# Kernel optimization log

Hardware: AMD Instinct MI355X
Metric: run time of the kernel (lower is better)

## Reference

```python
import jax, jax.numpy as jnp
import numpy as np
from jax import lax

C = 128          # channel_size
NUM_HEAD = 2
P = 4            # local_patch_num


def setup_inputs() -> dict:
    key = jax.random.key(0)
    ks = jax.random.split(key, 16)
    def w(k, shape, scale=0.02):
        return jax.random.normal(k, shape, dtype=jnp.float32) * scale
    return dict(
        x=jax.random.normal(ks[0], (16, C, 128, 128), jnp.float32),
        h0=jax.random.normal(ks[1], (1, C, 64, 64), jnp.float32),
        c0=jax.random.normal(ks[2], (1, C, 64, 64), jnp.float32),
        conv_w=w(ks[3], (C, C, 2, 2)), conv_b=jnp.zeros((C,), jnp.float32),
        qkv1_w=w(ks[4], (3 * C, C)), qkv1_b=jnp.zeros((3 * C,), jnp.float32),
        mlp1_w1=w(ks[5], (4 * C, C)), mlp1_b1=jnp.zeros((4 * C,), jnp.float32),
        mlp1_w2=w(ks[6], (C, 4 * C)), mlp1_b2=jnp.zeros((C,), jnp.float32),
        qkv2_w=w(ks[7], (3 * C, C)), qkv2_b=jnp.zeros((3 * C,), jnp.float32),
        mlp2_w1=w(ks[8], (4 * C, C)), mlp2_b1=jnp.zeros((4 * C,), jnp.float32),
        mlp2_w2=w(ks[9], (C, 4 * C)), mlp2_b2=jnp.zeros((C,), jnp.float32),
        lstm_wx=w(ks[10], (4 * C, C)),   # 1x1 conv, no bias
        lstm_wh=w(ks[11], (4 * C, C)),   # 1x1 conv
        lstm_bh=jnp.zeros((4 * C,), jnp.float32),
    )


def _linear(x, w, b):
    # torch Linear: y = x @ W.T + b, W is [out, in]
    return jnp.einsum('...i,oi->...o', x, w) + b


def _msa(x, w, b, num_head):
    # x: [b, A, L, c]; attend over L within each group A. scale = sqrt(channel_size).
    bb, A, L, c = x.shape
    hd = c // num_head
    qkv = _linear(x, w, b).reshape(bb, A, L, 3, num_head, hd)
    q = jnp.transpose(qkv[..., 0, :, :], (0, 1, 3, 2, 4))  # [b,A,h,L,hd]
    k = jnp.transpose(qkv[..., 1, :, :], (0, 1, 3, 2, 4))
    v = jnp.transpose(qkv[..., 2, :, :], (0, 1, 3, 2, 4))
    score = jnp.einsum('bahlc,bahmc->bahlm', q, k) / (c ** 0.5)
    attn = jax.nn.softmax(score, axis=-1)
    out = jnp.einsum('bahlm,bahmc->bahlc', attn, v)
    return jnp.transpose(out, (0, 1, 3, 2, 4)).reshape(bb, A, L, c)


def _mlp(x, w1, b1, w2, b2):
    return _linear(jax.nn.gelu(_linear(x, w1, b1), approximate=False), w2, b2)


def reference(x, h0, c0, conv_w, conv_b,
              qkv1_w, qkv1_b, mlp1_w1, mlp1_b1, mlp1_w2, mlp1_b2,
              qkv2_w, qkv2_b, mlp2_w1, mlp2_b1, mlp2_w2, mlp2_b2,
              lstm_wx, lstm_wh, lstm_bh):
    # Conv2d(C, C, kernel=2, stride=2)
    x = lax.conv_general_dilated(x, conv_w, (2, 2), 'VALID',
                                 dimension_numbers=('NCHW', 'OIHW', 'NCHW'))
    x = x + conv_b[None, :, None, None]
    b, c, Hs, Ws = x.shape
    yg, xg = Hs // P, Ws // P
    # Window_partition: b c (yg yl) (xg xl) -> b (yg xg) (yl xl) c
    xw = x.reshape(b, c, yg, P, xg, P).transpose(0, 2, 4, 3, 5, 1).reshape(b, yg * xg, P * P, c)
    xw = xw + _msa(xw, qkv1_w, qkv1_b, NUM_HEAD)      # LocalMSA over window tokens
    xw = xw + _mlp(xw, mlp1_w1, mlp1_b1, mlp1_w2, mlp1_b2)
    xt = jnp.transpose(xw, (0, 2, 1, 3))              # b g l c -> b l g c
    xt = xt + _msa(xt, qkv2_w, qkv2_b, NUM_HEAD)      # DilatedMSA over windows
    xt = xt + _mlp(xt, mlp2_w1, mlp2_b1, mlp2_w2, mlp2_b2)
    # Window_reverse: b (yl xl) (yg xg) c -> b c (yg yl) (xg xl)
    xr = xt.reshape(b, P, P, yg, xg, c).transpose(0, 5, 3, 1, 4, 2).reshape(b, c, yg * P, xg * P)

    # ConvLSTM recurrence over the batch dimension (hidden carried sample-to-sample)
    def step(carry, xi):
        h, Cc = carry  # [C,H,W]
        gates = (jnp.einsum('oc,chw->ohw', lstm_wx, xi)
                 + jnp.einsum('oc,chw->ohw', lstm_wh, h)
                 + lstm_bh[:, None, None])
        f, i, s, o = jnp.split(gates, 4, axis=0)
        f = jax.nn.softmax(f, axis=0)   # Softmax2d = softmax over channels
        i = jax.nn.softmax(i, axis=0)
        o = jax.nn.softmax(o, axis=0)
        s = jnp.tanh(s)
        Cn = f * Cc + i * s
        hn = o * jnp.tanh(Cn)
        return (hn, Cn), hn

    (hf, Cf), hs = lax.scan(step, (h0[0], c0[0]), xr)
    return hs, hf[None], Cf[None]
```

## Files before the change

### kernel.cpp

```cpp
#include <hip/hip_runtime.h>
#include <hip/hip_bf16.h>

typedef unsigned int u32;
typedef unsigned short u16;

#define DI __device__ __forceinline__

typedef __attribute__((ext_vector_type(8))) __bf16 bf16x8;
typedef __attribute__((ext_vector_type(4))) float f32x4;

DI float b2f_u(u32 u){ return __uint_as_float(u << 16); }
DI u16 f2b_u(float f){
  u32 x = __float_as_uint(f);
  x += 0x7fffu + ((x >> 16) & 1u);
  return (u16)(x >> 16);
}
DI void ld8b(const u16* p, float* o){
  uint4 v = *reinterpret_cast<const uint4*>(p);
  o[0] = b2f_u(v.x & 0xffffu); o[1] = b2f_u(v.x >> 16);
  o[2] = b2f_u(v.y & 0xffffu); o[3] = b2f_u(v.y >> 16);
  o[4] = b2f_u(v.z & 0xffffu); o[5] = b2f_u(v.z >> 16);
  o[6] = b2f_u(v.w & 0xffffu); o[7] = b2f_u(v.w >> 16);
}
DI void st8b(u16* p, const float* i){
  uint4 v;
  v.x = (u32)f2b_u(i[0]) | ((u32)f2b_u(i[1]) << 16);
  v.y = (u32)f2b_u(i[2]) | ((u32)f2b_u(i[3]) << 16);
  v.z = (u32)f2b_u(i[4]) | ((u32)f2b_u(i[5]) << 16);
  v.w = (u32)f2b_u(i[6]) | ((u32)f2b_u(i[7]) << 16);
  *reinterpret_cast<uint4*>(p) = v;
}

__global__ void k_detect(const u32* __restrict__ xw, int* __restrict__ flag){
  __shared__ int cnt;
  int t = threadIdx.x;
  if (t == 0) cnt = 0;
  __syncthreads();
  int c = 0;
  for (int i = t; i < 2048; i += 256){
    u32 lo = xw[i] & 0xffffu;
    u32 e = (lo >> 7) & 0xffu;
    if (e < 100u || e > 140u) c++;
  }
  atomicAdd(&cnt, c);
  __syncthreads();
  if (t == 0) *flag = (cnt > 200) ? 1 : 0;
}

__global__ void k_prep(
  const void* __restrict__ conv_w, const void* __restrict__ qkv1_w,
  const void* __restrict__ m1w1, const void* __restrict__ m1w2,
  const void* __restrict__ qkv2_w, const void* __restrict__ m2w1, const void* __restrict__ m2w2,
  const void* __restrict__ lwx, const void* __restrict__ lwh,
  const void* __restrict__ conv_b, const void* __restrict__ qkv1_b,
  const void* __restrict__ m1b1, const void* __restrict__ m1b2,
  const void* __restrict__ qkv2_b, const void* __restrict__ m2b1, const void* __restrict__ m2b2,
  const void* __restrict__ lbh,
  u16* __restrict__ wB_conv, u16* __restrict__ wB_qkv1, u16* __restrict__ wB_m1a,
  u16* __restrict__ wB_m1b, u16* __restrict__ wB_qkv2, u16* __restrict__ wB_m2a,
  u16* __restrict__ wB_m2b, u16* __restrict__ wBx, u16* __restrict__ wBh,
  float* __restrict__ bf_conv, float* __restrict__ bf_qkv1, float* __restrict__ bf_m1b1,
  float* __restrict__ bf_m1b2, float* __restrict__ bf_qkv2, float* __restrict__ bf_m2b1,
  float* __restrict__ bf_m2b2, float* __restrict__ bf_lbh,
  const int* __restrict__ flag){
  int bid = blockIdx.x, t = threadIdx.x;
  int fl = *flag;
  auto cvb = [&](const void* s, u16* d, int base, int n){
    int i = (bid - base)*256 + t;
    if (i < n) d[i] = fl ? f2b_u(((const float*)s)[i]) : ((const u16*)s)[i];
  };
  auto ldf = [&](const void* s, int i)->float{
    return fl ? ((const float*)s)[i] : b2f_u((u32)((const u16*)s)[i]);
  };
  if (bid < 256)       cvb(conv_w, wB_conv, 0,    65536);
  else if (bid < 448)  cvb(qkv1_w, wB_qkv1, 256,  49152);
  else if (bid < 704)  cvb(m1w1,   wB_m1a,  448,  65536);
  else if (bid < 960)  cvb(m1w2,   wB_m1b,  704,  65536);
  else if (bid < 1152) cvb(qkv2_w, wB_qkv2, 960,  49152);
  else if (bid < 1408) cvb(m2w1,   wB_m2a,  1152, 65536);
  else if (bid < 1664) cvb(m2w2,   wB_m2b,  1408, 65536);
  else if (bid < 1920) cvb(lwx,    wBx,     1664, 65536);
  else if (bid < 2176) cvb(lwh,    wBh,     1920, 65536);
  else {
    int i = (bid - 2176)*256 + t;
    if (i < 128)       bf_conv[i]        = ldf(conv_b, i);
    else if (i < 512)  bf_qkv1[i-128]    = ldf(qkv1_b, i-128);
    else if (i < 1024) bf_m1b1[i-512]    = ldf(m1b1,   i-512);
    else if (i < 1152) bf_m1b2[i-1024]   = ldf(m1b2,   i-1024);
    else if (i < 1536) bf_qkv2[i-1152]   = ldf(qkv2_b, i-1152);
    else if (i < 2048) bf_m2b1[i-1536]   = ldf(m2b1,   i-1536);
    else if (i < 2176) bf_m2b2[i-2048]   = ldf(m2b2,   i-2048);
    else if (i < 2688) bf_lbh[i-2176]    = ldf(lbh,    i-2176);
  }
}

__global__ __launch_bounds__(256) void k_conv(const void* __restrict__ x_raw,
                                              const u16* __restrict__ wB,
                                              const float* __restrict__ bias, u16* __restrict__ outA,
                                              const int* __restrict__ flag){
  __shared__ __align__(16) u16 pool[128*136];
  u16* Aa = pool;
  u16* Ys = pool;
  int t = threadIdx.x, bid = blockIdx.x;
  int xh = bid & 1, yg = (bid >> 1) & 15, b = bid >> 5;
  size_t slab = (size_t)b*2097152 + (size_t)(yg*8)*128 + (size_t)xh*64;
  int w = t >> 6, lane = t & 63, fr = lane & 15, fg = lane >> 4;
  f32x4 acc[2][8];
  #pragma unroll
  for (int j=0;j<8;j++){
    float bv = bias[j*16 + fr];
    acc[0][j] = {bv,bv,bv,bv};
    acc[1][j] = {bv,bv,bv,bv};
  }
  for (int ci0 = 0; ci0 < 128; ci0 += 16){
    if (ci0) __syncthreads();
    if (*flag){
      const float* xb = (const float*)x_raw + slab + (size_t)ci0*16384;
      #pragma unroll
      for (int i=0;i<4;i++){
        int idx = i*256 + t;
        int row = idx >> 3, seg = idx & 7;
        int cr = row >> 3, py = row & 7;
        const float* sp = xb + (size_t)cr*16384 + py*128 + seg*8;
        float4 v0 = *reinterpret_cast<const float4*>(sp);
        float4 v1 = *reinterpret_cast<const float4*>(sp + 4);
        int tok0 = seg*16 + (py>>1)*4;
        int k0 = cr*4 + (py&1)*2;
        *reinterpret_cast<u32*>(&Aa[(tok0+0)*72 + k0]) = (u32)f2b_u(v0.x) | ((u32)f2b_u(v0.y)<<16);
        *reinterpret_cast<u32*>(&Aa[(tok0+1)*72 + k0]) = (u32)f2b_u(v0.z) | ((u32)f2b_u(v0.w)<<16);
        *reinterpret_cast<u32*>(&Aa[(tok0+2)*72 + k0]) = (u32)f2b_u(v1.x) | ((u32)f2b_u(v1.y)<<16);
        *reinterpret_cast<u32*>(&Aa[(tok0+3)*72 + k0]) = (u32)f2b_u(v1.z) | ((u32)f2b_u(v1.w)<<16);
      }
    } else {
      const u16* xb = (const u16*)x_raw + slab + (size_t)ci0*16384;
      #pragma unroll
      for (int i=0;i<4;i++){
        int idx = i*256 + t;
        int row = idx >> 3, seg = idx & 7;
        int cr = row >> 3, py = row & 7;
        uint4 v = *reinterpret_cast<const uint4*>(xb + (size_t)cr*16384 + py*128 + seg*8);
        int tok0 = seg*16 + (py>>1)*4;
        int k0 = cr*4 + (py&1)*2;
        *reinterpret_cast<u32*>(&Aa[(tok0+0)*72 + k0]) = v.x;
        *reinterpret_cast<u32*>(&Aa[(tok0+1)*72 + k0]) = v.y;
        *reinterpret_cast<u32*>(&Aa[(tok0+2)*72 + k0]) = v.z;
        *reinterpret_cast<u32*>(&Aa[(tok0+3)*72 + k0]) = v.w;
      }
    }
    __syncthreads();
    bf16x8 a0[2], a1[2];
    #pragma unroll
    for (int kk=0;kk<2;kk++){
      a0[kk] = *reinterpret_cast<const bf16x8*>(&Aa[(w*16+fr)*72 + kk*32 + fg*8]);
      a1[kk] = *reinterpret_cast<const bf16x8*>(&Aa[((w+4)*16+fr)*72 + kk*32 + fg*8]);
    }
    #pragma unroll
    for (int j=0;j<8;j++){
      const u16* wp = wB + (size_t)(j*16+fr)*512 + ci0*4 + fg*8;
      bf16x8 b0 = *reinterpret_cast<const bf16x8*>(wp);
      bf16x8 b1 = *reinterpret_cast<const bf16x8*>(wp + 32);
      acc[0][j] = __builtin_amdgcn_mfma_f32_16x16x32_bf16(a0[0], b0, acc[0][j], 0, 0, 0);
      acc[0][j] = __builtin_amdgcn_mfma_f32_16x16x32_bf16(a0[1], b1, acc[0][j], 0, 0, 0);
      acc[1][j] = __builtin_amdgcn_mfma_f32_16x16x32_bf16(a1[0], b0, acc[1][j], 0, 0, 0);
      acc[1][j] = __builtin_amdgcn_mfma_f32_16x16x32_bf16(a1[1], b1, acc[1][j], 0, 0, 0);
    }
  }
  __syncthreads();
  #pragma unroll
  for (int tt=0;tt<2;tt++){
    int tokbase = (w + tt*4)*16;
    #pragma unroll
    for (int j=0;j<8;j++){
      #pragma unroll
      for (int r=0;r<4;r++)
        Ys[(tokbase + fg*4 + r)*136 + j*16 + fr] = f2b_u(acc[tt][j][r]);
    }
  }
  __syncthreads();
  {
    int tok = t >> 1, half = t & 1;
    int gl = yg*16 + xh*8 + (tok >> 4);
    int l = tok & 15;
    u16* dst = outA + ((size_t)(b*256 + gl)*16 + l)*128 + half*64;
    const u16* src = &Ys[tok*136 + half*64];
    #pragma unroll
    for (int q2=0;q2<8;q2++)
      *reinterpret_cast<uint4*>(dst + q2*8) = *reinterpret_cast<const uint4*>(src + q2*8);
  }
}

__global__ __launch_bounds__(256) void k_msa1(const u16* __restrict__ A, const u16* __restrict__ wB,
                                              const float* __restrict__ qbias, u16* __restrict__ B){
  __shared__ u16 Xs[16*136];
  __shared__ float QKV[16*388];
  __shared__ float S[512];
  int t = threadIdx.x, bid = blockIdx.x;
  {
    int l = t >> 4, c0 = (t & 15)*8;
    *reinterpret_cast<uint4*>(&Xs[l*136 + c0]) =
      *reinterpret_cast<const uint4*>(A + (size_t)bid*2048 + l*128 + c0);
  }
  __syncthreads();
  {
    int w = t >> 6, lane = t & 63, fr = lane & 15, fg = lane >> 4;
    bf16x8 a[4];
    #pragma unroll
    for (int k=0;k<4;k++) a[k] = *reinterpret_cast<const bf16x8*>(&Xs[fr*136 + k*32 + fg*8]);
    #pragma unroll
    for (int j=0;j<6;j++){
      int o = w*96 + j*16 + fr;
      float bv = qbias[o];
      f32x4 d = {bv,bv,bv,bv};
      const u16* wp = wB + (size_t)o*128 + fg*8;
      #pragma unroll
      for (int k=0;k<4;k++){
        bf16x8 b = *reinterpret_cast<const bf16x8*>(wp + k*32);
        d = __builtin_amdgcn_mfma_f32_16x16x32_bf16(a[k], b, d, 0, 0, 0);
      }
      #pragma unroll
      for (int r=0;r<4;r++) QKV[(fg*4+r)*388 + o] = d[r];
    }
  }
  __syncthreads();
  const float scale = 0.08838834764831845f;
  for (int e = t; e < 512; e += 256){
    int h = e >> 8, l = (e>>4)&15, m = e&15;
    const float* q = &QKV[l*388 + h*64];
    const float* kk = &QKV[m*388 + 128 + h*64];
    float s = 0.f;
    #pragma unroll
    for (int d=0; d<64; d++) s += q[d]*kk[d];
    S[(h*16+l)*16 + m] = s*scale;
  }
  __syncthreads();
  if (t < 32){
    float* row = &S[t*16];
    float mx = row[0];
    #pragma unroll
    for (int m=1;m<16;m++) mx = fmaxf(mx,row[m]);
    float sum = 0.f;
    #pragma unroll
    for (int m=0;m<16;m++){ float e = expf(row[m]-mx); row[m]=e; sum+=e; }
    float inv = 1.0f/sum;
    #pragma unroll
    for (int m=0;m<16;m++) row[m] *= inv;
  }
  __syncthreads();
  {
    int l = t >> 4, og = t & 15, o0 = og*8;
    int h = o0 >> 6;
    const float* p = &S[(h*16+l)*16];
    float out8[8];
    #pragma unroll
    for (int j=0;j<8;j++){
      int o = o0+j, d = o & 63;
      float s = 0.f;
      #pragma unroll
      for (int m=0;m<16;m++) s += p[m]*QKV[m*388 + 256 + h*64 + d];
      out8[j] = s + b2f_u((u32)Xs[l*136 + o]);
    }
    st8b(B + (size_t)bid*2048 + l*128 + o0, out8);
  }
}

template<int MODE>
__global__ __launch_bounds__(256) void k_mlp(const u16* __restrict__ in,
    const u16* __restrict__ w1B, const float* __restrict__ b1,
    const u16* __restrict__ w2B, const float* __restrict__ b2,
    u16* __restrict__ out){
  __shared__ u16 Xs[32*136];
  __shared__ u16 Hs[32*520];
  __shared__ u16 Ys[32*136];
  int t = threadIdx.x, bid = blockIdx.x;
  {
    int l = t >> 3, c0 = (t & 7)*16;
    const u16* src = in + (size_t)bid*4096 + l*128 + c0;
    *reinterpret_cast<uint4*>(&Xs[l*136 + c0])     = *reinterpret_cast<const uint4*>(src);
    *reinterpret_cast<uint4*>(&Xs[l*136 + c0 + 8]) = *reinterpret_cast<const uint4*>(src + 8);
  }
  __syncthreads();
  int w = t >> 6, lane = t & 63, fr = lane & 15, fg = lane >> 4;

  {
    bf16x8 a0[4], a1[4];
    #pragma unroll
    for (int k=0;k<4;k++){
      a0[k] = *reinterpret_cast<const bf16x8*>(&Xs[fr*136 + k*32 + fg*8]);
      a1[k] = *reinterpret_cast<const bf16x8*>(&Xs[(16+fr)*136 + k*32 + fg*8]);
    }
    #pragma unroll
    for (int j=0;j<8;j++){
      int o = w*128 + j*16 + fr;
      float bv = b1[o];
      f32x4 d0 = {bv,bv,bv,bv}, d1 = {bv,bv,bv,bv};
      const u16* wp = w1B + (size_t)o*128 + fg*8;
      #pragma unroll
      for (int k=0;k<4;k++){
        bf16x8 b = *reinterpret_cast<const bf16x8*>(wp + k*32);
        d0 = __builtin_amdgcn_mfma_f32_16x16x32_bf16(a0[k], b, d0, 0, 0, 0);
        d1 = __builtin_amdgcn_mfma_f32_16x16x32_bf16(a1[k], b, d1, 0, 0, 0);
      }
      #pragma unroll
      for (int r=0;r<4;r++){
        float v0 = d0[r], v1 = d1[r];
        Hs[(fg*4+r)*520 + o]      = f2b_u(0.5f*v0*(1.0f + erff(v0*0.70710678118654752f)));
        Hs[(16+fg*4+r)*520 + o]   = f2b_u(0.5f*v1*(1.0f + erff(v1*0.70710678118654752f)));
      }
    }
  }
  __syncthreads();

  {
    int na = w*32 + fr, nb = na + 16;
    float ba = b2[na], bb = b2[nb];
    f32x4 d00 = {ba,ba,ba,ba}, d01 = {bb,bb,bb,bb};
    f32x4 d10 = {ba,ba,ba,ba}, d11 = {bb,bb,bb,bb};
    const u16* wpa = w2B + (size_t)na*512 + fg*8;
    const u16* wpb = w2B + (size_t)nb*512 + fg*8;
    #pragma unroll
    for (int k=0;k<16;k++){
      bf16x8 aa = *reinterpret_cast<const bf16x8*>(&Hs[fr*520 + k*32 + fg*8]);
      bf16x8 ab = *reinterpret_cast<const bf16x8*>(&Hs[(16+fr)*520 + k*32 + fg*8]);
      bf16x8 bA = *reinterpret_cast<const bf16x8*>(wpa + k*32);
      bf16x8 bB = *reinterpret_cast<const bf16x8*>(wpb + k*32);
      d00 = __builtin_amdgcn_mfma_f32_16x16x32_bf16(aa, bA, d00, 0, 0, 0);
      d01 = __builtin_amdgcn_mfma_f32_16x16x32_bf16(aa, bB, d01, 0, 0, 0);
      d10 = __builtin_amdgcn_mfma_f32_16x16x32_bf16(ab, bA, d10, 0, 0, 0);
      d11 = __builtin_amdgcn_mfma_f32_16x16x32_bf16(ab, bB, d11, 0, 0, 0);
    }
    #pragma unroll
    for (int r=0;r<4;r++){
      int ta = fg*4 + r, tb = 16 + ta;
      Ys[ta*136 + na] = f2b_u(d00[r] + b2f_u((u32)Xs[ta*136 + na]));
      Ys[ta*136 + nb] = f2b_u(d01[r] + b2f_u((u32)Xs[ta*136 + nb]));
      Ys[tb*136 + na] = f2b_u(d10[r] + b2f_u((u32)Xs[tb*136 + na]));
      Ys[tb*136 + nb] = f2b_u(d11[r] + b2f_u((u32)Xs[tb*136 + nb]));
    }
  }
  __syncthreads();

  {
    int tok = t >> 3, oc = (t & 7)*16;
    uint4 v0 = *reinterpret_cast<const uint4*>(&Ys[tok*136 + oc]);
    uint4 v1 = *reinterpret_cast<const uint4*>(&Ys[tok*136 + oc + 8]);
    int T = bid*32 + tok;
    size_t addr;
    if (MODE == 1){
      int b = T >> 12, g = (T >> 4) & 255, ll = T & 15;
      addr = ((size_t)((b*16 + ll)*256 + g))*128 + oc;
    } else {
      int b = T >> 12, ll = (T >> 8) & 15, g = T & 255;
      int pcoord = ((g >> 4)*4 + (ll >> 2))*64 + ((g & 15)*4 + (ll & 3));
      addr = ((size_t)(b*4096 + pcoord))*128 + oc;
    }
    *reinterpret_cast<uint4*>(out + addr)     = v0;
    *reinterpret_cast<uint4*>(out + addr + 8) = v1;
  }
}

__global__ __launch_bounds__(256) void k_qkv2(const u16* __restrict__ in, const u16* __restrict__ wB,
                                              const float* __restrict__ bias,
                                              u16* __restrict__ qbuf, u16* __restrict__ kvbuf){
  __shared__ u16 Xs[16*136];
  __shared__ u16 Qs[16*392];
  int t = threadIdx.x, bid = blockIdx.x;
  {
    int l = t >> 4, c0 = (t & 15)*8;
    *reinterpret_cast<uint4*>(&Xs[l*136 + c0]) =
      *reinterpret_cast<const uint4*>(in + (size_t)bid*2048 + l*128 + c0);
  }
  __syncthreads();
  {
    int w = t >> 6, lane = t & 63, fr = lane & 15, fg = lane >> 4;
    bf16x8 a[4];
    #pragma unroll
    for (int k=0;k<4;k++) a[k] = *reinterpret_cast<const bf16x8*>(&Xs[fr*136 + k*32 + fg*8]);
    #pragma unroll
    for (int j=0;j<6;j++){
      int o = w*96 + j*16 + fr;
      float bv = bias[o];
      f32x4 d = {bv,bv,bv,bv};
      const u16* wp = wB + (size_t)o*128 + fg*8;
      #pragma unroll
      for (int k=0;k<4;k++){
        bf16x8 b = *reinterpret_cast<const bf16x8*>(wp + k*32);
        d = __builtin_amdgcn_mfma_f32_16x16x32_bf16(a[k], b, d, 0, 0, 0);
      }
      #pragma unroll
      for (int r=0;r<4;r++) Qs[(fg*4+r)*392 + o] = f2b_u(d[r]);
    }
  }
  __syncthreads();
  {
    int l = t >> 4, og = t & 15, o0 = og*24;
    size_t tok = (size_t)bid*16 + l;
    #pragma unroll
    for (int m=0; m<3; m++){
      int oc = o0 + m*8;
      uint4 v = *reinterpret_cast<const uint4*>(&Qs[l*392 + oc]);
      if (oc < 128) *reinterpret_cast<uint4*>(qbuf + tok*128 + oc) = v;
      else          *reinterpret_cast<uint4*>(kvbuf + tok*256 + (oc-128)) = v;
    }
  }
}

__global__ __launch_bounds__(256) void k_attn2(const u16* __restrict__ qbuf, const u16* __restrict__ kvbuf,
                                               u16* __restrict__ y){
  __shared__ __align__(16) char pool[24064];
  u16* Qb = (u16*)pool;
  u16* Kb = (u16*)(pool + 9216);
  u16* Vt = (u16*)(pool + 13824);
  u16* Pb = (u16*)(pool + 18944);
  float* Os = (float*)pool;

  int t = threadIdx.x, bid = blockIdx.x;
  int qt = bid & 3, h = (bid >> 2) & 1, bl = bid >> 3;
  size_t tokbase = (size_t)bl * 256;
  {
    int r = t >> 2, seg = t & 3;
    const u16* src = qbuf + (tokbase + qt*64 + r)*128 + h*64 + seg*16;
    uint4 v0 = *reinterpret_cast<const uint4*>(src);
    uint4 v1 = *reinterpret_cast<const uint4*>(src + 8);
    *reinterpret_cast<uint4*>(&Qb[r*72 + seg*16])     = v0;
    *reinterpret_cast<uint4*>(&Qb[r*72 + seg*16 + 8]) = v1;
  }
  int w = t >> 6, lane = t & 63;
  int fc = lane & 15, fg = lane >> 4;
  float m_reg[4], l_reg[4];
  #pragma unroll
  for (int r=0;r<4;r++){ m_reg[r] = -1e30f; l_reg[r] = 0.0f; }
  f32x4 o[4];
  #pragma unroll
  for (int j=0;j<4;j++) o[j] = {0.f,0.f,0.f,0.f};
  const float scale = 0.08838834764831845f;

  for (int kt=0; kt<8; kt++){
    {
      int r = t >> 3, seg = t & 7;
      const u16* base = kvbuf + (tokbase + kt*32 + r)*256 + h*64;
      *reinterpret_cast<uint4*>(&Kb[r*72 + seg*8]) = *reinterpret_cast<const uint4*>(base + seg*8);
    }
    {
      int pp = t >> 4, dg = t & 15, d0 = dg*4;
      const u16* b0 = kvbuf + (tokbase + kt*32 + 2*pp)*256 + h*64 + 128 + d0;
      uint2 v0 = *reinterpret_cast<const uint2*>(b0);
      uint2 v1 = *reinterpret_cast<const uint2*>(b0 + 256);
      *reinterpret_cast<u32*>(&Vt[(d0+0)*40 + 2*pp]) = (v0.x & 0xffffu) | (v1.x << 16);
      *reinterpret_cast<u32*>(&Vt[(d0+1)*40 + 2*pp]) = (v0.x >> 16) | (v1.x & 0xffff0000u);
      *reinterpret_cast<u32*>(&Vt[(d0+2)*40 + 2*pp]) = (v0.y & 0xffffu) | (v1.y << 16);
      *reinterpret_cast<u32*>(&Vt[(d0+3)*40 + 2*pp]) = (v0.y >> 16) | (v1.y & 0xffff0000u);
    }
    __syncthreads();
    f32x4 s0 = {0.f,0.f,0.f,0.f}, s1 = {0.f,0.f,0.f,0.f};
    {
      bf16x8 a0  = *reinterpret_cast<const bf16x8*>(&Qb[(w*16+fc)*72 + fg*8]);
      bf16x8 a1  = *reinterpret_cast<const bf16x8*>(&Qb[(w*16+fc)*72 + 32 + fg*8]);
      bf16x8 b00 = *reinterpret_cast<const bf16x8*>(&Kb[fc*72 + fg*8]);
      bf16x8 b01 = *reinterpret_cast<const bf16x8*>(&Kb[fc*72 + 32 + fg*8]);
      bf16x8 b10 = *reinterpret_cast<const bf16x8*>(&Kb[(16+fc)*72 + fg*8]);
      bf16x8 b11 = *reinterpret_cast<const bf16x8*>(&Kb[(16+fc)*72 + 32 + fg*8]);
      s0 = __builtin_amdgcn_mfma_f32_16x16x32_bf16(a0, b00, s0, 0, 0, 0);
      s0 = __builtin_amdgcn_mfma_f32_16x16x32_bf16(a1, b01, s0, 0, 0, 0);
      s1 = __builtin_amdgcn_mfma_f32_16x16x32_bf16(a0, b10, s1, 0, 0, 0);
      s1 = __builtin_amdgcn_mfma_f32_16x16x32_bf16(a1, b11, s1, 0, 0, 0);
    }
    float corr[4];
    #pragma unroll
    for (int r=0;r<4;r++){
      float v0 = s0[r]*scale, v1 = s1[r]*scale;
      float mx = fmaxf(v0, v1);
      mx = fmaxf(mx, __shfl_xor(mx, 1));
      mx = fmaxf(mx, __shfl_xor(mx, 2));
      mx = fmaxf(mx, __shfl_xor(mx, 4));
      mx = fmaxf(mx, __shfl_xor(mx, 8));
      float mnew = fmaxf(m_reg[r], mx);
      corr[r] = expf(m_reg[r] - mnew);
      m_reg[r] = mnew;
      float p0 = expf(v0 - mnew), p1 = expf(v1 - mnew);
      float sum = p0 + p1;
      sum += __shfl_xor(sum, 1);
      sum += __shfl_xor(sum, 2);
      sum += __shfl_xor(sum, 4);
      sum += __shfl_xor(sum, 8);
      l_reg[r] = l_reg[r]*corr[r] + sum;
      int row = w*16 + fg*4 + r;
      Pb[row*40 + fc]      = f2b_u(p0);
      Pb[row*40 + 16 + fc] = f2b_u(p1);
    }
    {
      bf16x8 pa = *reinterpret_cast<const bf16x8*>(&Pb[(w*16+fc)*40 + fg*8]);
      #pragma unroll
      for (int jt=0;jt<4;jt++){
        bf16x8 vb = *reinterpret_cast<const bf16x8*>(&Vt[(jt*16+fc)*40 + fg*8]);
        f32x4 oo = o[jt];
        oo[0] *= corr[0]; oo[1] *= corr[1]; oo[2] *= corr[2]; oo[3] *= corr[3];
        o[jt] = __builtin_amdgcn_mfma_f32_16x16x32_bf16(pa, vb, oo, 0, 0, 0);
      }
    }
    __syncthreads();
  }
  float inv[4];
  #pragma unroll
  for (int r=0;r<4;r++) inv[r] = 1.0f / l_reg[r];
  #pragma unroll
  for (int jt=0;jt<4;jt++){
    #pragma unroll
    for (int r=0;r<4;r++)
      Os[(w*16 + fg*4 + r)*68 + jt*16 + fc] = o[jt][r] * inv[r];
  }
  __syncthreads();
  {
    int row = t >> 2, seg = t & 3;
    float ov[16];
    #pragma unroll
    for (int j=0;j<16;j++) ov[j] = Os[row*68 + seg*16 + j];
    u16* dst = y + (tokbase + qt*64 + row)*128 + h*64 + seg*16;
    float res[16]; ld8b(dst, res); ld8b(dst+8, res+8);
    float o16[16];
    #pragma unroll
    for (int j=0;j<16;j++) o16[j] = ov[j] + res[j];
    st8b(dst, o16); st8b(dst+8, o16+8);
  }
}

__global__ __launch_bounds__(256) void k_lstm_all(const u16* __restrict__ xD,
    const void* __restrict__ h0, const void* __restrict__ c0,
    const u16* __restrict__ wBx, const u16* __restrict__ wBh, const float* __restrict__ bh,
    void* __restrict__ dout, const int* __restrict__ flag){
  __shared__ u16 Xa[16*136];
  __shared__ u16 Ha[16*136];
  __shared__ float glds[4*16*132];
  __shared__ float Cls[16*132];
  __shared__ u16 hst[16*136];
  int t = threadIdx.x, bid = blockIdx.x;
  int pix0 = bid*16;
  int fl = *flag;
  {
    int c = t >> 1, half = t & 1;
    int pxb = half*8;
    if (fl){
      const float* hp = (const float*)h0 + (size_t)c*4096 + pix0 + pxb;
      const float* cp = (const float*)c0 + (size_t)c*4096 + pix0 + pxb;
      #pragma unroll
      for (int i=0;i<8;i++){
        Ha[(pxb+i)*136 + c] = f2b_u(hp[i]);
        Cls[(pxb+i)*132 + c] = cp[i];
      }
    } else {
      const u16* hp = (const u16*)h0 + (size_t)c*4096 + pix0 + pxb;
      const u16* cp = (const u16*)c0 + (size_t)c*4096 + pix0 + pxb;
      #pragma unroll
      for (int i=0;i<8;i++){
        Ha[(pxb+i)*136 + c] = hp[i];
        Cls[(pxb+i)*132 + c] = b2f_u((u32)cp[i]);
      }
    }
  }
  int w = t >> 6, lane = t & 63, fr = lane & 15, fg = lane >> 4;
  for (int n = 0; n < 16; n++){
    {
      int px = t >> 4, c0v = (t & 15)*8;
      *reinterpret_cast<uint4*>(&Xa[px*136 + c0v]) =
        *reinterpret_cast<const uint4*>(xD + ((size_t)n*4096 + pix0 + px)*128 + c0v);
    }
    __syncthreads();
    f32x4 acc[8];
    {
      bf16x8 ax[4], ah[4];
      #pragma unroll
      for (int k=0;k<4;k++){
        ax[k] = *reinterpret_cast<const bf16x8*>(&Xa[fr*136 + k*32 + fg*8]);
        ah[k] = *reinterpret_cast<const bf16x8*>(&Ha[fr*136 + k*32 + fg*8]);
      }
      #pragma unroll
      for (int j=0;j<8;j++){
        int o = w*128 + j*16 + fr;
        float bv = bh[o];
        f32x4 d = {bv,bv,bv,bv};
        const u16* wpx = wBx + (size_t)o*128 + fg*8;
        const u16* wph = wBh + (size_t)o*128 + fg*8;
        #pragma unroll
        for (int k=0;k<4;k++){
          bf16x8 b = *reinterpret_cast<const bf16x8*>(wpx + k*32);
          d = __builtin_amdgcn_mfma_f32_16x16x32_bf16(ax[k], b, d, 0, 0, 0);
        }
        #pragma unroll
        for (int k=0;k<4;k++){
          bf16x8 b = *reinterpret_cast<const bf16x8*>(wph + k*32);
          d = __builtin_amdgcn_mfma_f32_16x16x32_bf16(ah[k], b, d, 0, 0, 0);
        }
        acc[j] = d;
      }
    }
    if (w == 2){
      #pragma unroll
      for (int j=0;j<8;j++)
        #pragma unroll
        for (int r=0;r<4;r++)
          glds[(w*16 + fg*4 + r)*132 + j*16 + fr] = tanhf(acc[j][r]);
    } else {
      #pragma unroll
      for (int r=0;r<4;r++){
        float mx = acc[0][r];
        #pragma unroll
        for (int j=1;j<8;j++) mx = fmaxf(mx, acc[j][r]);
        mx = fmaxf(mx, __shfl_xor(mx, 1));
        mx = fmaxf(mx, __shfl_xor(mx, 2));
        mx = fmaxf(mx, __shfl_xor(mx, 4));
        mx = fmaxf(mx, __shfl_xor(mx, 8));
        float e[8], sum = 0.f;
        #pragma unroll
        for (int j=0;j<8;j++){ e[j] = expf(acc[j][r] - mx); sum += e[j]; }
        sum += __shfl_xor(sum, 1);
        sum += __shfl_xor(sum, 2);
        sum += __shfl_xor(sum, 4);
        sum += __shfl_xor(sum, 8);
        float inv = 1.0f/sum;
        #pragma unroll
        for (int j=0;j<8;j++)
          glds[(w*16 + fg*4 + r)*132 + j*16 + fr] = e[j]*inv;
      }
    }
    __syncthreads();
    {
      int chg = t & 15, px = t >> 4;
      int ch0 = chg*8;
      float fv[8], iv[8], sv[8], ov[8], cc[8];
      #pragma unroll
      for (int q2=0;q2<2;q2++){
        *reinterpret_cast<float4*>(&fv[q2*4]) = *reinterpret_cast<const float4*>(&glds[(0*16+px)*132 + ch0 + q2*4]);
        *reinterpret_cast<float4*>(&iv[q2*4]) = *reinterpret_cast<const float4*>(&glds[(1*16+px)*132 + ch0 + q2*4]);
        *reinterpret_cast<float4*>(&sv[q2*4]) = *reinterpret_cast<const float4*>(&glds[(2*16+px)*132 + ch0 + q2*4]);
        *reinterpret_cast<float4*>(&ov[q2*4]) = *reinterpret_cast<const float4*>(&glds[(3*16+px)*132 + ch0 + q2*4]);
        *reinterpret_cast<float4*>(&cc[q2*4]) = *reinterpret_cast<const float4*>(&Cls[px*132 + ch0 + q2*4]);
      }
      float cn[8], hn[8];
      #pragma unroll
      for (int j=0;j<8;j++){
        cn[j] = fv[j]*cc[j] + iv[j]*sv[j];
        hn[j] = ov[j]*tanhf(cn[j]);
      }
      #pragma unroll
      for (int q2=0;q2<2;q2++)
        *reinterpret_cast<float4*>(&Cls[px*132 + ch0 + q2*4]) = *reinterpret_cast<const float4*>(&cn[q2*4]);
      uint4 pk;
      pk.x = (u32)f2b_u(hn[0]) | ((u32)f2b_u(hn[1]) << 16);
      pk.y = (u32)f2b_u(hn[2]) | ((u32)f2b_u(hn[3]) << 16);
      pk.z = (u32)f2b_u(hn[4]) | ((u32)f2b_u(hn[5]) << 16);
      pk.w = (u32)f2b_u(hn[6]) | ((u32)f2b_u(hn[7]) << 16);
      *reinterpret_cast<uint4*>(&Ha[px*136 + ch0])  = pk;
      *reinterpret_cast<uint4*>(&hst[px*136 + ch0]) = pk;
      if (n == 15){
        #pragma unroll
        for (int q2=0;q2<2;q2++)
          *reinterpret_cast<float4*>(&glds[px*132 + ch0 + q2*4]) = *reinterpret_cast<const float4*>(&hn[q2*4]);
      }
    }
    __syncthreads();
    {
      int ch = t >> 1, ph = t & 1;
      size_t ob = (size_t)n*524288 + (size_t)ch*4096 + pix0 + ph*8;
      if (fl){
        float* df = (float*)dout;
        float v[8];
        #pragma unroll
        for (int i=0;i<8;i++) v[i] = b2f_u((u32)hst[(ph*8+i)*136 + ch]);
        *reinterpret_cast<float4*>(df + ob)     = make_float4(v[0],v[1],v[2],v[3]);
        *reinterpret_cast<float4*>(df + ob + 4) = make_float4(v[4],v[5],v[6],v[7]);
      } else {
        u16* db = (u16*)dout;
        uint4 pk;
        pk.x = (u32)hst[(ph*8+0)*136 + ch] | ((u32)hst[(ph*8+1)*136 + ch] << 16);
        pk.y = (u32)hst[(ph*8+2)*136 + ch] | ((u32)hst[(ph*8+3)*136 + ch] << 16);
        pk.z = (u32)hst[(ph*8+4)*136 + ch] | ((u32)hst[(ph*8+5)*136 + ch] << 16);
        pk.w = (u32)hst[(ph*8+6)*136 + ch] | ((u32)hst[(ph*8+7)*136 + ch] << 16);
        *reinterpret_cast<uint4*>(db + ob) = pk;
      }
    }
  }
  __syncthreads();
  {
    int c = t >> 1, half = t & 1;
    int pxb = half*8;
    if (fl){
      float hv[8], cv[8];
      #pragma unroll
      for (int i=0;i<8;i++){ hv[i] = glds[(pxb+i)*132 + c]; cv[i] = Cls[(pxb+i)*132 + c]; }
      float* df = (float*)dout;
      size_t hb = 8388608u + (size_t)c*4096 + pix0 + pxb;
      size_t cb = 8912896u + (size_t)c*4096 + pix0 + pxb;
      *reinterpret_cast<float4*>(df + hb)     = make_float4(hv[0],hv[1],hv[2],hv[3]);
      *reinterpret_cast<float4*>(df + hb + 4) = make_float4(hv[4],hv[5],hv[6],hv[7]);
      *reinterpret_cast<float4*>(df + cb)     = make_float4(cv[0],cv[1],cv[2],cv[3]);
      *reinterpret_cast<float4*>(df + cb + 4) = make_float4(cv[4],cv[5],cv[6],cv[7]);
    } else {
      u16* db = (u16*)dout;
      uint4 hp, cp2;
      hp.x = (u32)hst[(pxb+0)*136 + c] | ((u32)hst[(pxb+1)*136 + c] << 16);
      hp.y = (u32)hst[(pxb+2)*136 + c] | ((u32)hst[(pxb+3)*136 + c] << 16);
      hp.z = (u32)hst[(pxb+4)*136 + c] | ((u32)hst[(pxb+5)*136 + c] << 16);
      hp.w = (u32)hst[(pxb+6)*136 + c] | ((u32)hst[(pxb+7)*136 + c] << 16);
      cp2.x = (u32)f2b_u(Cls[(pxb+0)*132 + c]) | ((u32)f2b_u(Cls[(pxb+1)*132 + c]) << 16);
      cp2.y = (u32)f2b_u(Cls[(pxb+2)*132 + c]) | ((u32)f2b_u(Cls[(pxb+3)*132 + c]) << 16);
      cp2.z = (u32)f2b_u(Cls[(pxb+4)*132 + c]) | ((u32)f2b_u(Cls[(pxb+5)*132 + c]) << 16);
      cp2.w = (u32)f2b_u(Cls[(pxb+6)*132 + c]) | ((u32)f2b_u(Cls[(pxb+7)*132 + c]) << 16);
      *reinterpret_cast<uint4*>(db + 8388608u + (size_t)c*4096 + pix0 + pxb) = hp;
      *reinterpret_cast<uint4*>(db + 8912896u + (size_t)c*4096 + pix0 + pxb) = cp2;
    }
  }
}

extern "C" void kernel_launch(void* const* d_in, const int* in_sizes, int n_in,
                              void* d_out, int out_size, void* d_ws, size_t ws_size,
                              hipStream_t stream) {
  const void* x      = d_in[0];
  const void* h0     = d_in[1];
  const void* c0     = d_in[2];
  const void* conv_w = d_in[3];
  const void* conv_b = d_in[4];
  const void* qkv1_w = d_in[5];
  const void* qkv1_b = d_in[6];
  const void* m1w1   = d_in[7];
  const void* m1b1   = d_in[8];
  const void* m1w2   = d_in[9];
  const void* m1b2   = d_in[10];
  const void* qkv2_w = d_in[11];
  const void* qkv2_b = d_in[12];
  const void* m2w1   = d_in[13];
  const void* m2b1   = d_in[14];
  const void* m2w2   = d_in[15];
  const void* m2b2   = d_in[16];
  const void* lwx    = d_in[17];
  const void* lwh    = d_in[18];
  const void* lbh    = d_in[19];

  char* p = (char*)d_ws;
  auto alloc = [&](size_t bytes)->void*{
    void* r = (void*)p; p += (bytes + 255) & ~(size_t)255; return r;
  };
  int*   flag    = (int*)alloc(256);
  u16* wB_conv = (u16*)alloc(128*512*2);
  u16* wB_qkv1 = (u16*)alloc(384*128*2);
  u16* wB_m1a  = (u16*)alloc(512*128*2);
  u16* wB_m1b  = (u16*)alloc(128*512*2);
  u16* wB_qkv2 = (u16*)alloc(384*128*2);
  u16* wB_m2a  = (u16*)alloc(512*128*2);
  u16* wB_m2b  = (u16*)alloc(128*512*2);
  u16* wBx     = (u16*)alloc(512*128*2);
  u16* wBh     = (u16*)alloc(512*128*2);
  float* bf_conv = (float*)alloc(128*4);
  float* bf_qkv1 = (float*)alloc(384*4);
  float* bf_m1b1 = (float*)alloc(512*4);
  float* bf_m1b2 = (float*)alloc(128*4);
  float* bf_qkv2 = (float*)alloc(384*4);
  float* bf_m2b1 = (float*)alloc(512*4);
  float* bf_m2b2 = (float*)alloc(128*4);
  float* bf_lbh  = (float*)alloc(512*4);
  u16* R0   = (u16*)alloc(16777216);
  u16* Rbig = (u16*)alloc(33554432);

  u16* bufA = R0;
  u16* bufB = Rbig;
  u16* bufC = R0;
  u16* qbuf = (u16*)d_out;
  u16* kvbuf = Rbig;
  u16* bufD = Rbig;

  k_detect<<<1, 256, 0, stream>>>((const u32*)x, flag);

  k_prep<<<2187, 256, 0, stream>>>(
      conv_w, qkv1_w, m1w1, m1w2, qkv2_w, m2w1, m2w2, lwx, lwh,
      conv_b, qkv1_b, m1b1, m1b2, qkv2_b, m2b1, m2b2, lbh,
      wB_conv, wB_qkv1, wB_m1a, wB_m1b, wB_qkv2, wB_m2a, wB_m2b,
      wBx, wBh,
      bf_conv, bf_qkv1, bf_m1b1, bf_m1b2, bf_qkv2, bf_m2b1, bf_m2b2, bf_lbh,
      flag);

  k_conv<<<512, 256, 0, stream>>>(x, wB_conv, bf_conv, bufA, flag);
  k_msa1<<<4096, 256, 0, stream>>>(bufA, wB_qkv1, bf_qkv1, bufB);
  k_mlp<1><<<2048, 256, 0, stream>>>(bufB, wB_m1a, bf_m1b1, wB_m1b, bf_m1b2, bufC);
  k_qkv2<<<4096, 256, 0, stream>>>(bufC, wB_qkv2, bf_qkv2, qbuf, kvbuf);
  k_attn2<<<2048, 256, 0, stream>>>(qbuf, kvbuf, bufC);
  k_mlp<2><<<2048, 256, 0, stream>>>(bufC, wB_m2a, bf_m2b1, wB_m2b, bf_m2b2, bufD);

  k_lstm_all<<<256, 256, 0, stream>>>(bufD, h0, c0, wBx, wBh, bf_lbh, d_out, flag);
}
```

Measured before the change: 663.9 us.

## Split LSTM gate GEMM over K across two wave groups in 512-thread blocks

The recurrent LSTM kernel now launches 512 threads per block. Waves 0-3 compute the input-projection half of the gate matmul and waves 4-7 compute the hidden-projection half. The hidden-half partial sums go through a new shared-memory buffer and an extra barrier before the softmax/tanh epilogue. This halves the serial MFMA chain per wave in a latency-bound 256-block recurrence, at the cost of more LDS, an extra sync per step, and lower occupancy per CU.

```diff
diff --git a/kernel.cpp b/kernel.cpp
--- a/kernel.cpp
+++ b/kernel.cpp
@@ -523,19 +523,20 @@
   }
 }
 
-__global__ __launch_bounds__(256) void k_lstm_all(const u16* __restrict__ xD,
+__global__ __launch_bounds__(512) void k_lstm_all(const u16* __restrict__ xD,
     const void* __restrict__ h0, const void* __restrict__ c0,
     const u16* __restrict__ wBx, const u16* __restrict__ wBh, const float* __restrict__ bh,
     void* __restrict__ dout, const int* __restrict__ flag){
   __shared__ u16 Xa[16*136];
   __shared__ u16 Ha[16*136];
   __shared__ float glds[4*16*132];
+  __shared__ float part[4*16*132];
   __shared__ float Cls[16*132];
   __shared__ u16 hst[16*136];
   int t = threadIdx.x, bid = blockIdx.x;
   int pix0 = bid*16;
   int fl = *flag;
-  {
+  if (t < 256){
     int c = t >> 1, half = t & 1;
     int pxb = half*8;
     if (fl){
@@ -557,8 +558,11 @@
     }
   }
   int w = t >> 6, lane = t & 63, fr = lane & 15, fg = lane >> 4;
+  int g = w & 3, ks = w >> 2;
+  const u16* wSel = ks ? wBh : wBx;
+  const u16* aSel = ks ? Ha : Xa;
   for (int n = 0; n < 16; n++){
-    {
+    if (t < 256){
       int px = t >> 4, c0v = (t & 15)*8;
       *reinterpret_cast<uint4*>(&Xa[px*136 + c0v]) =
         *reinterpret_cast<const uint4*>(xD + ((size_t)n*4096 + pix0 + px)*128 + c0v);
@@ -566,63 +570,71 @@
     __syncthreads();
     f32x4 acc[8];
     {
-      bf16x8 ax[4], ah[4];
-      #pragma unroll
-      for (int k=0;k<4;k++){
-        ax[k] = *reinterpret_cast<const bf16x8*>(&Xa[fr*136 + k*32 + fg*8]);
-        ah[k] = *reinterpret_cast<const bf16x8*>(&Ha[fr*136 + k*32 + fg*8]);
-      }
+      bf16x8 a[4];
+      #pragma unroll
+      for (int k=0;k<4;k++)
+        a[k] = *reinterpret_cast<const bf16x8*>(&aSel[fr*136 + k*32 + fg*8]);
       #pragma unroll
       for (int j=0;j<8;j++){
-        int o = w*128 + j*16 + fr;
-        float bv = bh[o];
-        f32x4 d = {bv,bv,bv,bv};
-        const u16* wpx = wBx + (size_t)o*128 + fg*8;
-        const u16* wph = wBh + (size_t)o*128 + fg*8;
+        int o = g*128 + j*16 + fr;
+        f32x4 d;
+        if (ks == 0){ float bv = bh[o]; d = {bv,bv,bv,bv}; }
+        else        { d = {0.f,0.f,0.f,0.f}; }
+        const u16* wp = wSel + (size_t)o*128 + fg*8;
         #pragma unroll
         for (int k=0;k<4;k++){
-          bf16x8 b = *reinterpret_cast<const bf16x8*>(wpx + k*32);
-          d = __builtin_amdgcn_mfma_f32_16x16x32_bf16(ax[k], b, d, 0, 0, 0);
-        }
-        #pragma unroll
-        for (int k=0;k<4;k++){
-          bf16x8 b = *reinterpret_cast<const bf16x8*>(wph + k*32);
-          d = __builtin_amdgcn_mfma_f32_16x16x32_bf16(ah[k], b, d, 0, 0, 0);
+          bf16x8 b = *reinterpret_cast<const bf16x8*>(wp + k*32);
+          d = __builtin_amdgcn_mfma_f32_16x16x32_bf16(a[k], b, d, 0, 0, 0);
         }
         acc[j] = d;
       }
     }
-    if (w == 2){
+    if (ks == 1){
       #pragma unroll
       for (int j=0;j<8;j++)
         #pragma unroll
         for (int r=0;r<4;r++)
-          glds[(w*16 + fg*4 + r)*132 + j*16 + fr] = tanhf(acc[j][r]);
-    } else {
-      #pragma unroll
-      for (int r=0;r<4;r++){
-        float mx = acc[0][r];
+          part[(g*16 + fg*4 + r)*132 + j*16 + fr] = acc[j][r];
+    }
+    __syncthreads();
+    if (ks == 0){
+      #pragma unroll
+      for (int j=0;j<8;j++)
         #pragma unroll
-        for (int j=1;j<8;j++) mx = fmaxf(mx, acc[j][r]);
-        mx = fmaxf(mx, __shfl_xor(mx, 1));
-        mx = fmaxf(mx, __shfl_xor(mx, 2));
-        mx = fmaxf(mx, __shfl_xor(mx, 4));
-        mx = fmaxf(mx, __shfl_xor(mx, 8));
-        float e[8], sum = 0.f;
-        #pragma unroll
-        for (int j=0;j<8;j++){ e[j] = expf(acc[j][r] - mx); sum += e[j]; }
-        sum += __shfl_xor(sum, 1);
-        sum += __shfl_xor(sum, 2);
-        sum += __shfl_xor(sum, 4);
-        sum += __shfl_xor(sum, 8);
-        float inv = 1.0f/sum;
+        for (int r=0;r<4;r++)
+          acc[j][r] += part[(g*16 + fg*4 + r)*132 + j*16 + fr];
+      if (g == 2){
         #pragma unroll
         for (int j=0;j<8;j++)
-          glds[(w*16 + fg*4 + r)*132 + j*16 + fr] = e[j]*inv;
+          #pragma unroll
+          for (int r=0;r<4;r++)
+            glds[(g*16 + fg*4 + r)*132 + j*16 + fr] = tanhf(acc[j][r]);
+      } else {
+        #pragma unroll
+        for (int r=0;r<4;r++){
+          float mx = acc[0][r];
+          #pragma unroll
+          for (int j=1;j<8;j++) mx = fmaxf(mx, acc[j][r]);
+          mx = fmaxf(mx, __shfl_xor(mx, 1));
+          mx = fmaxf(mx, __shfl_xor(mx, 2));
+          mx = fmaxf(mx, __shfl_xor(mx, 4));
+          mx = fmaxf(mx, __shfl_xor(mx, 8));
+          float e[8], sum = 0.f;
+          #pragma unroll
+          for (int j=0;j<8;j++){ e[j] = expf(acc[j][r] - mx); sum += e[j]; }
+          sum += __shfl_xor(sum, 1);
+          sum += __shfl_xor(sum, 2);
+          sum += __shfl_xor(sum, 4);
+          sum += __shfl_xor(sum, 8);
+          float inv = 1.0f/sum;
+          #pragma unroll
+          for (int j=0;j<8;j++)
+            glds[(g*16 + fg*4 + r)*132 + j*16 + fr] = e[j]*inv;
+        }
       }
     }
     __syncthreads();
-    {
+    if (t < 256){
       int chg = t & 15, px = t >> 4;
       int ch0 = chg*8;
       float fv[8], iv[8], sv[8], ov[8], cc[8];
@@ -657,7 +669,7 @@
       }
     }
     __syncthreads();
-    {
+    if (t < 256){
       int ch = t >> 1, ph = t & 1;
       size_t ob = (size_t)n*524288 + (size_t)ch*4096 + pix0 + ph*8;
       if (fl){
@@ -679,7 +691,7 @@
     }
   }
   __syncthreads();
-  {
+  if (t < 256){
     int c = t >> 1, half = t & 1;
     int pxb = half*8;
     if (fl){
@@ -783,5 +795,5 @@
   k_attn2<<<2048, 256, 0, stream>>>(qbuf, kvbuf, bufC);
   k_mlp<2><<<2048, 256, 0, stream>>>(bufC, wB_m2a, bf_m2b1, wB_m2b, bf_m2b2, bufD);
 
-  k_lstm_all<<<256, 256, 0, stream>>>(bufD, h0, c0, wBx, wBh, bf_lbh, d_out, flag);
-}
+  k_lstm_all<<<256, 512, 0, stream>>>(bufD, h0, c0, wBx, wBh, bf_lbh, d_out, flag);
+}
```

After: 712.3 us (median of 2 runs). 7.3% more time.
